# Optimization experiments

Hardware: AMD Instinct MI355X
Metric: run time of the kernel (lower is better)

## Reference

```python
import jax, jax.numpy as jnp
import numpy as np
from jax import lax

BT, ST, NT = 32, 8, 1024
CH = [128, 64, 32, 16, 8]
DIL = [1, 2, 4, 8, 16]
K = 5
EPS = 1e-5


def setup_inputs() -> dict:
    key = jax.random.key(0)
    ks = jax.random.split(key, 32)
    inp = {}
    inp["x"] = jax.random.normal(ks[0], (BT, ST, CH[0], NT), jnp.float32)
    nt_out = NT * 32  # 5 x2 upsamples
    inp["targets"] = jax.random.uniform(ks[1], (BT, 3, nt_out, ST), dtype=jnp.float32)
    for i in range(4):
        inp[f"w{i}"] = jax.random.normal(ks[2 + i], (CH[i + 1], CH[i], K), jnp.float32) * 0.05
        inp[f"g{i}"] = 1.0 + 0.1 * jax.random.normal(ks[6 + i], (CH[i + 1],), jnp.float32)
        inp[f"b{i}"] = 0.1 * jax.random.normal(ks[10 + i], (CH[i + 1],), jnp.float32)
        inp[f"m{i}"] = 0.1 * jax.random.normal(ks[14 + i], (CH[i + 1],), jnp.float32)
        inp[f"v{i}"] = 0.5 + 0.5 * jax.random.uniform(ks[18 + i], (CH[i + 1],), dtype=jnp.float32)
    inp["w_out"] = jax.random.normal(ks[22], (3, CH[4], K), jnp.float32) * 0.05
    inp["b_out"] = jax.random.normal(ks[23], (3,), jnp.float32) * 0.05
    return inp


def _conv(x, w, d):
    # reflect-padded dilated conv1d, same length out (torch padding_mode='reflect')
    p = ((K - 1) * d + 1) // 2
    xp = jnp.pad(x, ((0, 0), (0, 0), (p, p)), mode="reflect")
    return lax.conv_general_dilated(xp, w, window_strides=(1,), padding="VALID",
                                    rhs_dilation=(d,),
                                    dimension_numbers=("NCH", "OIH", "NCH"))


def _up2(x):
    # F.interpolate(scale_factor=2, mode='linear', align_corners=False)
    L = x.shape[-1]
    coords = (jnp.arange(2 * L, dtype=jnp.float32) + 0.5) / 2.0 - 0.5
    coords = jnp.clip(coords, 0.0, L - 1.0)
    i0 = jnp.floor(coords).astype(jnp.int32)
    i1 = jnp.minimum(i0 + 1, L - 1)
    w = coords - i0.astype(jnp.float32)
    return x[..., i0] * (1.0 - w) + x[..., i1] * w


def _forward(x, targets, ws, gs, bs, ms, vs, w_out, b_out):
    h = x.reshape(BT * ST, CH[0], NT)
    for i in range(4):
        h = _conv(h, ws[i], DIL[i])
        inv = gs[i] / jnp.sqrt(vs[i] + EPS)
        h = h * inv[None, :, None] + (bs[i] - ms[i] * inv)[None, :, None]  # eval-mode BN
        h = jax.nn.relu(h)
        h = _up2(h)
    h = _conv(h, w_out, DIL[4]) + b_out[None, :, None]
    h = _up2(h)
    out = h.reshape(BT, ST, 3, h.shape[-1]).transpose(0, 2, 3, 1)  # [bt, 3, nt_out, st]
    # vectorized equivalent of the per-(i,j) Python loop counting non-all-zero targets
    mask = jnp.any(targets != 0, axis=(1, 2))  # [bt, st]
    num = jnp.sum(mask).astype(jnp.float32)
    loss = jnp.sum(-targets * jax.nn.log_softmax(out, axis=1)) / (num * targets.shape[2])
    return out, loss


def reference(x, targets, w0, w1, w2, w3, g0, g1, g2, g3, b0, b1, b2, b3,
              m0, m1, m2, m3, v0, v1, v2, v3, w_out, b_out):
    return _forward(x, targets, [w0, w1, w2, w3], [g0, g1, g2, g3],
                    [b0, b1, b2, b3], [m0, m1, m2, m3], [v0, v1, v2, v3],
                    w_out, b_out)
```

## Files before the change

### kernel.cpp

```cpp
#include <hip/hip_runtime.h>
#include <hip/hip_bf16.h>
#include <cstdint>
#include <cstddef>

#define K5 5
#define BNEPS 1e-5f

typedef __attribute__((ext_vector_type(8))) short short8v;
typedef __attribute__((ext_vector_type(4))) short short4v;
typedef __attribute__((ext_vector_type(4))) float float4v;

struct __attribute__((packed, aligned(4))) f4u { float4v v; };

__device__ inline float bf2f(short s) {
    __hip_bfloat16 h = *(__hip_bfloat16*)&s;
    return __bfloat162float(h);
}
__device__ inline short f2bf(float f) {
    __hip_bfloat16 h = __float2bfloat16(f);
    return *(short*)&h;
}

template<int CIN, int COUT, int MROWS, int KPAD>
__device__ inline void wprep_body(const float* __restrict__ w,
                                  short* __restrict__ wb, int blk, int tid) {
    int idx = blk * 256 + tid;
    if (idx >= MROWS * KPAD) return;
    int co = idx / KPAD, kk = idx - co * KPAD;
    int tap = kk / CIN, ci = kk & (CIN - 1);
    float v = (co < COUT && tap < K5) ? w[((size_t)co * CIN + ci) * K5 + tap] : 0.f;
    wb[idx] = f2bf(v);
}

__global__ __launch_bounds__(256) void wprep_all_ker(
    const float* __restrict__ w0, const float* __restrict__ w1,
    const float* __restrict__ w2, const float* __restrict__ w3,
    const float* __restrict__ w4,
    short* __restrict__ wb0, short* __restrict__ wb1, short* __restrict__ wb2,
    short* __restrict__ wb3, short* __restrict__ wb4) {
    int b = blockIdx.x, t = threadIdx.x;
    if (b < 160)      wprep_body<128, 64, 64, 640>(w0, wb0, b, t);
    else if (b < 200) wprep_body<64, 32, 32, 320>(w1, wb1, b - 160, t);
    else if (b < 210) wprep_body<32, 16, 16, 160>(w2, wb2, b - 200, t);
    else if (b < 216) wprep_body<16, 8, 16, 96>(w3, wb3, b - 210, t);
    else              wprep_body<8, 3, 16, 64>(w4, wb4, b - 216, t);
}

template<int CIN, int COUT, int DIL, int LOUT, int T_TILE, int WT,
         bool HAS_BN, int IN_MODE, int OUT_MODE>
__global__ __launch_bounds__(256) void conv_ker(
    const void* __restrict__ in_, const short* __restrict__ wb,
    const float* __restrict__ gg, const float* __restrict__ bb,
    const float* __restrict__ mm, const float* __restrict__ vv,
    void* __restrict__ out_)
{
    constexpr int P = 2 * DIL;
    constexpr int XT = T_TILE + 4 * DIL;
    constexpr int ROWW = CIN + 8;
    constexpr int K = CIN * K5;
    constexpr int KPAD = ((K + 31) / 32) * 32;
    constexpr int NSTEP = KPAD / 32;
    constexpr int WCOT = (COUT + 15) / 16;
    constexpr int TN = T_TILE / (16 * WT);
    constexpr int LIN = LOUT;
    constexpr int LIN_BASE = (IN_MODE == 1) ? (LOUT / 2) : LOUT;
    static_assert(T_TILE % (16 * WT) == 0, "tile split");

    __shared__ short sx[XT * ROWW];
    __shared__ float ssc[COUT], ssh[COUT];

    const int n = blockIdx.x;
    const int t0 = blockIdx.y * T_TILE;
    const int tid = threadIdx.x;

    if (tid < COUT) {
        if constexpr (HAS_BN) {
            float inv = gg[tid] * rsqrtf(vv[tid] + BNEPS);
            ssc[tid] = inv;
            ssh[tid] = bb[tid] - mm[tid] * inv;
        } else {
            ssc[tid] = 1.f;
            ssh[tid] = bb[tid];
        }
    }

    if constexpr (IN_MODE == 0) {
        static_assert(XT % 4 == 0, "XT mult of 4");
        constexpr int T4 = XT / 4;
        constexpr int NITEM = T4 * (CIN / 8);
        const float* in = (const float*)in_;
        for (int uidx = tid; uidx < NITEM; uidx += 256) {
            int t4 = uidx % T4;
            int ci0 = (uidx / T4) * 8;
            const int u0 = t0 - P + 4 * t4;
            const float* base = in + ((size_t)n * CIN + ci0) * LIN_BASE;
            short8v rows[4];
            bool fast = (u0 >= 0) && (u0 + 3 <= LIN - 1);
            if (fast) {
#pragma unroll
                for (int j = 0; j < 8; ++j) {
                    f4u xv = *(const f4u*)(base + (size_t)j * LIN_BASE + u0);
#pragma unroll
                    for (int r = 0; r < 4; ++r) rows[r][j] = f2bf(xv.v[r]);
                }
            } else {
#pragma unroll
                for (int r = 0; r < 4; ++r) {
                    int u = u0 + r;
                    u = (u < 0) ? -u : u;
                    u = (u >= LIN) ? (2 * (LIN - 1) - u) : u;
#pragma unroll
                    for (int j = 0; j < 8; ++j)
                        rows[r][j] = f2bf(base[(size_t)j * LIN_BASE + u]);
                }
            }
            short* dst = sx + (4 * t4) * ROWW + ci0;
            *(short8v*)(dst) = rows[0];
            *(short8v*)(dst + ROWW) = rows[1];
            *(short8v*)(dst + 2 * ROWW) = rows[2];
            *(short8v*)(dst + 3 * ROWW) = rows[3];
        }
    } else {
        constexpr int CPR = CIN / 8;
        const short* inb = (const short*)in_ + (size_t)n * LIN_BASE * CIN;
        for (int uidx = tid; uidx < XT * CPR; uidx += 256) {
            int ci0 = (uidx % CPR) * 8;
            int t = uidx / CPR;
            int u = t0 - P + t;
            u = (u < 0) ? -u : u;
            u = (u >= LIN) ? (2 * (LIN - 1) - u) : u;
            int i = u >> 1;
            int ia, ib; float wa, wbw;
            if (u & 1) { ia = i; ib = (i + 1 < LIN_BASE) ? i + 1 : LIN_BASE - 1; wa = 0.75f; wbw = 0.25f; }
            else if (i == 0) { ia = 0; ib = 0; wa = 1.0f; wbw = 0.0f; }
            else { ia = i - 1; ib = i; wa = 0.25f; wbw = 0.75f; }
            short8v va = *(const short8v*)(inb + (size_t)ia * CIN + ci0);
            short8v vb = *(const short8v*)(inb + (size_t)ib * CIN + ci0);
            short8v pack;
#pragma unroll
            for (int j = 0; j < 8; ++j) {
                short sa = va[j], sb = vb[j];
                pack[j] = f2bf(wa * bf2f(sa) + wbw * bf2f(sb));
            }
            *(short8v*)(sx + t * ROWW + ci0) = pack;
        }
    }
    __syncthreads();

    const int wvi = tid >> 6;
    const int lane = tid & 63;
    const int ln = lane & 15;
    const int q = lane >> 4;
    const int tw = wvi * (TN * 16);

    float4v acc[WCOT][TN];
#pragma unroll
    for (int c = 0; c < WCOT; ++c)
#pragma unroll
        for (int j = 0; j < TN; ++j)
            acc[c][j] = (float4v){0.f, 0.f, 0.f, 0.f};

    const short* arow[WCOT];
#pragma unroll
    for (int c = 0; c < WCOT; ++c)
        arow[c] = wb + ((size_t)(c * 16 + ln)) * KPAD + q * 8;

    short8v acur[WCOT], anx[WCOT];
#pragma unroll
    for (int c = 0; c < WCOT; ++c)
        acur[c] = *(const short8v*)(arow[c]);

#pragma unroll 1
    for (int s = 0; s < NSTEP; ++s) {
        if (s + 1 < NSTEP) {
#pragma unroll
            for (int c = 0; c < WCOT; ++c)
                anx[c] = *(const short8v*)(arow[c] + (s + 1) * 32);
        }
        const int kk = s * 32 + q * 8;
        int tap = kk / CIN;
        const int ci0 = kk & (CIN - 1);
        if constexpr (KPAD != K) {
            tap = (tap < K5) ? tap : (K5 - 1);
        }
        short8v b[TN];
#pragma unroll
        for (int j = 0; j < TN; ++j)
            b[j] = *(const short8v*)(sx + (tw + j * 16 + ln + tap * DIL) * ROWW + ci0);
        if constexpr (KPAD != K) {
            if (kk >= K) {
                short8v z = {0, 0, 0, 0, 0, 0, 0, 0};
#pragma unroll
                for (int j = 0; j < TN; ++j) b[j] = z;
            }
        }
#pragma unroll
        for (int c = 0; c < WCOT; ++c)
#pragma unroll
            for (int j = 0; j < TN; ++j)
                acc[c][j] = __builtin_amdgcn_mfma_f32_16x16x32_bf16(acur[c], b[j], acc[c][j], 0, 0, 0);
#pragma unroll
        for (int c = 0; c < WCOT; ++c)
            acur[c] = anx[c];
    }

    if constexpr (OUT_MODE == 0) {
        short* ob = (short*)out_ + ((size_t)n * LOUT + t0 + tw) * COUT;
#pragma unroll
        for (int c = 0; c < WCOT; ++c)
#pragma unroll
            for (int j = 0; j < TN; ++j) {
                if ((COUT % 16 == 0) || (q * 4 + 3 < COUT)) {
                    float4v v = acc[c][j];
                    short4v pk;
#pragma unroll
                    for (int r = 0; r < 4; ++r) {
                        int co = c * 16 + q * 4 + r;
                        float val = v[r] * ssc[co] + ssh[co];
                        if constexpr (HAS_BN) val = fmaxf(val, 0.f);
                        pk[r] = f2bf(val);
                    }
                    *(short4v*)(ob + (size_t)(j * 16 + ln) * COUT + c * 16 + q * 4) = pk;
                }
            }
    } else {
        float* ob = (float*)out_ + (size_t)n * COUT * LOUT + t0 + tw + ln;
#pragma unroll
        for (int c = 0; c < WCOT; ++c)
#pragma unroll
            for (int j = 0; j < TN; ++j) {
                float4v v = acc[c][j];
#pragma unroll
                for (int r = 0; r < 4; ++r) {
                    int co = c * 16 + q * 4 + r;
                    if ((COUT % 16 == 0) || co < COUT) {
                        float val = v[r] * ssc[co] + ssh[co];
                        if constexpr (HAS_BN) val = fmaxf(val, 0.f);
                        ob[(size_t)co * LOUT + j * 16] = val;
                    }
                }
            }
    }
}

__global__ __launch_bounds__(256) void up_loss_ker(
    const float* __restrict__ h4, const float* __restrict__ targets,
    float* __restrict__ out, float* __restrict__ loss_sum, int* __restrict__ flags)
{
    constexpr int L = 16384, LO = 32768;
    const int bt = blockIdx.x;
    const int t0 = blockIdx.y * 256;
    const int tid = threadIdx.x;
    const int i0 = t0 >> 1;

    __shared__ float sh[3 * 8 * 132];
    __shared__ int snz[8];
    __shared__ float swv[4];

    {
        const bool interior = (i0 >= 1) && (i0 + 130 <= L - 1);
        for (int idx = tid; idx < 24 * 33; idx += 256) {
            int row = idx / 33;
            int qd = idx - row * 33;
            int c = row >> 3, s = row & 7;
            int nn = bt * 8 + s;
            const float* src = h4 + ((size_t)nn * 3 + c) * L;
            int bi0 = i0 - 1 + 4 * qd;
            float4v v;
            if (interior) {
                v = ((const f4u*)(src + bi0))->v;
            } else {
#pragma unroll
                for (int k = 0; k < 4; ++k) {
                    int bi = bi0 + k;
                    bi = bi < 0 ? 0 : (bi > L - 1 ? L - 1 : bi);
                    v[k] = src[bi];
                }
            }
            *(float4v*)(sh + row * 132 + 4 * qd) = v;
        }
    }
    if (tid < 8) snz[tid] = 0;
    __syncthreads();

    const int tl = tid >> 1;
    const int st4 = (tid & 1) * 4;

    float lsum = 0.f;
    int nzm = 0;
#pragma unroll
    for (int rr = 0; rr < 2; ++rr) {
        int t = t0 + rr * 128 + tl;
        int li = (t >> 1) - i0 + 1;
        float o[3][4];
#pragma unroll
        for (int c = 0; c < 3; ++c)
#pragma unroll
            for (int s = 0; s < 4; ++s) {
                const float* row = sh + ((c << 3) + st4 + s) * 132;
                float v;
                if (t & 1) v = 0.75f * row[li] + 0.25f * row[li + 1];
                else       v = 0.25f * row[li - 1] + 0.75f * row[li];
                o[c][s] = v;
            }
        float tg[3][4];
#pragma unroll
        for (int c = 0; c < 3; ++c) {
            size_t obase = (((size_t)bt * 3 + c) * LO + t) * 8 + st4;
            float4v ov = { o[c][0], o[c][1], o[c][2], o[c][3] };
            *(float4v*)(out + obase) = ov;
            float4v tv = *(const float4v*)(targets + obase);
            tg[c][0] = tv[0]; tg[c][1] = tv[1]; tg[c][2] = tv[2]; tg[c][3] = tv[3];
        }
#pragma unroll
        for (int s = 0; s < 4; ++s) {
            float a0 = o[0][s], a1 = o[1][s], a2 = o[2][s];
            float mx = fmaxf(a0, fmaxf(a1, a2));
            float e0 = __expf(a0 - mx), e1 = __expf(a1 - mx), e2 = __expf(a2 - mx);
            float lse = mx + __logf(e0 + e1 + e2);
            lsum += tg[0][s] * (lse - a0) + tg[1][s] * (lse - a1) + tg[2][s] * (lse - a2);
            if ((tg[0][s] != 0.f) | (tg[1][s] != 0.f) | (tg[2][s] != 0.f)) nzm |= 1 << s;
        }
    }
    if (nzm) {
#pragma unroll
        for (int s = 0; s < 4; ++s) if (nzm & (1 << s)) snz[st4 + s] = 1;
    }

#pragma unroll
    for (int off = 32; off > 0; off >>= 1) lsum += __shfl_down(lsum, off, 64);
    if ((tid & 63) == 0) swv[tid >> 6] = lsum;
    __syncthreads();
    if (tid == 0) atomicAdd(loss_sum, swv[0] + swv[1] + swv[2] + swv[3]);
    if (tid < 8 && snz[tid]) atomicOr(&flags[bt * 8 + tid], 1);
}

__global__ __launch_bounds__(256) void finalize_ker(
    const int* __restrict__ flags, const float* __restrict__ loss_sum,
    float* __restrict__ out_loss)
{
    __shared__ int s[256];
    s[threadIdx.x] = flags[threadIdx.x] ? 1 : 0;
    __syncthreads();
    for (int off = 128; off > 0; off >>= 1) {
        if (threadIdx.x < off) s[threadIdx.x] += s[threadIdx.x + off];
        __syncthreads();
    }
    if (threadIdx.x == 0) out_loss[0] = loss_sum[0] / ((float)s[0] * 32768.0f);
}

extern "C" void kernel_launch(void* const* d_in, const int* in_sizes, int n_in,
                              void* d_out, int out_size, void* d_ws, size_t ws_size,
                              hipStream_t stream)
{
    const float* x  = (const float*)d_in[0];
    const float* tg = (const float*)d_in[1];
    const float* w0 = (const float*)d_in[2];
    const float* g0 = (const float*)d_in[3];
    const float* b0 = (const float*)d_in[4];
    const float* m0 = (const float*)d_in[5];
    const float* v0 = (const float*)d_in[6];
    const float* w1 = (const float*)d_in[7];
    const float* g1 = (const float*)d_in[8];
    const float* b1 = (const float*)d_in[9];
    const float* m1 = (const float*)d_in[10];
    const float* v1 = (const float*)d_in[11];
    const float* w2 = (const float*)d_in[12];
    const float* g2 = (const float*)d_in[13];
    const float* b2 = (const float*)d_in[14];
    const float* m2 = (const float*)d_in[15];
    const float* v2 = (const float*)d_in[16];
    const float* w3 = (const float*)d_in[17];
    const float* g3 = (const float*)d_in[18];
    const float* b3 = (const float*)d_in[19];
    const float* m3 = (const float*)d_in[20];
    const float* v3 = (const float*)d_in[21];
    const float* w_out = (const float*)d_in[22];
    const float* b_out = (const float*)d_in[23];
    float* outp = (float*)d_out;

    char* ws = (char*)d_ws;
    int* flags = (int*)ws;
    float* loss_sum = (float*)(ws + 1024);
    short* wb0 = (short*)(ws + 4096);
    short* wb1 = (short*)(ws + 86016);
    short* wb2 = (short*)(ws + 106496);
    short* wb3 = (short*)(ws + 111616);
    short* wb4 = (short*)(ws + 114688);
    const size_t BUF_OFF = 131072;
    const size_t BUFN = (size_t)16777216;
    float* bufA = (float*)(ws + BUF_OFF);
    float* bufB = (ws_size >= BUF_OFF + 2 * BUFN * 4)
                      ? (bufA + BUFN)
                      : (float*)d_out;

    hipMemsetAsync(d_ws, 0, 4096, stream);

    wprep_all_ker<<<220, 256, 0, stream>>>(w0, w1, w2, w3, w_out,
                                           wb0, wb1, wb2, wb3, wb4);

    conv_ker<128, 64, 1, 1024, 128, 4, true, 0, 0>
        <<<dim3(256, 8), 256, 0, stream>>>(x, wb0, g0, b0, m0, v0, bufA);
    conv_ker<64, 32, 2, 2048, 128, 4, true, 1, 0>
        <<<dim3(256, 16), 256, 0, stream>>>(bufA, wb1, g1, b1, m1, v1, bufB);
    conv_ker<32, 16, 4, 4096, 256, 4, true, 1, 0>
        <<<dim3(256, 16), 256, 0, stream>>>(bufB, wb2, g2, b2, m2, v2, bufA);
    conv_ker<16, 8, 8, 8192, 256, 4, true, 1, 0>
        <<<dim3(256, 32), 256, 0, stream>>>(bufA, wb3, g3, b3, m3, v3, bufB);
    conv_ker<8, 3, 16, 16384, 256, 4, false, 1, 1>
        <<<dim3(256, 64), 256, 0, stream>>>(bufB, wb4, b_out, b_out, b_out, b_out, bufA);
    up_loss_ker<<<dim3(32, 128), 256, 0, stream>>>(bufA, tg, outp, loss_sum, flags);
    finalize_ker<<<1, 256, 0, stream>>>(flags, loss_sum, outp + (size_t)(out_size - 1));
}
```

Before: 561.7 us.

## Split conv waves across output-channel groups, enlarge time tiles, preload weights

Adds a WCO template parameter so the four waves of a block can be split between time and output-channel groups. The first two layers use a 2x2 split, which shrinks each wave's accumulator set and lets it cover more time positions. Time tiles are enlarged for layers 1-4 so fewer blocks recompute the dilated halo. Short K loops now load all weight fragments up front, and long loops prefetch two steps ahead. The cost is larger LDS tiles and more registers per wave, which can lower occupancy, and the CIN=8 row stride is padded to 24.

Result: faster. 511.0 us (-9.0%).

```diff
diff --git a/kernel.cpp b/kernel.cpp
--- a/kernel.cpp
+++ b/kernel.cpp
@@ -46,7 +46,7 @@
     else              wprep_body<8, 3, 16, 64>(w4, wb4, b - 216, t);
 }
 
-template<int CIN, int COUT, int DIL, int LOUT, int T_TILE, int WT,
+template<int CIN, int COUT, int DIL, int LOUT, int T_TILE, int WT, int WCO,
          bool HAS_BN, int IN_MODE, int OUT_MODE>
 __global__ __launch_bounds__(256) void conv_ker(
     const void* __restrict__ in_, const short* __restrict__ wb,
@@ -56,14 +56,17 @@
 {
     constexpr int P = 2 * DIL;
     constexpr int XT = T_TILE + 4 * DIL;
-    constexpr int ROWW = CIN + 8;
+    constexpr int ROWW = (CIN == 8) ? 24 : (CIN + 8);
     constexpr int K = CIN * K5;
     constexpr int KPAD = ((K + 31) / 32) * 32;
     constexpr int NSTEP = KPAD / 32;
-    constexpr int WCOT = (COUT + 15) / 16;
+    constexpr int MT = (COUT + 15) / 16;
+    constexpr int CT = MT / WCO;
     constexpr int TN = T_TILE / (16 * WT);
     constexpr int LIN = LOUT;
     constexpr int LIN_BASE = (IN_MODE == 1) ? (LOUT / 2) : LOUT;
+    static_assert(WT * WCO == 4, "4 waves");
+    static_assert(MT % WCO == 0, "co split");
     static_assert(T_TILE % (16 * WT) == 0, "tile split");
 
     __shared__ short sx[XT * ROWW];
@@ -151,63 +154,98 @@
     const int lane = tid & 63;
     const int ln = lane & 15;
     const int q = lane >> 4;
-    const int tw = wvi * (TN * 16);
-
-    float4v acc[WCOT][TN];
-#pragma unroll
-    for (int c = 0; c < WCOT; ++c)
+    const int tg = wvi % WT;
+    const int cg = wvi / WT;
+    const int tw = tg * (TN * 16);
+
+    float4v acc[CT][TN];
+#pragma unroll
+    for (int c = 0; c < CT; ++c)
 #pragma unroll
         for (int j = 0; j < TN; ++j)
             acc[c][j] = (float4v){0.f, 0.f, 0.f, 0.f};
 
-    const short* arow[WCOT];
-#pragma unroll
-    for (int c = 0; c < WCOT; ++c)
-        arow[c] = wb + ((size_t)(c * 16 + ln)) * KPAD + q * 8;
-
-    short8v acur[WCOT], anx[WCOT];
-#pragma unroll
-    for (int c = 0; c < WCOT; ++c)
-        acur[c] = *(const short8v*)(arow[c]);
-
+    const short* arow[CT];
+#pragma unroll
+    for (int c = 0; c < CT; ++c)
+        arow[c] = wb + ((size_t)((cg * CT + c) * 16 + ln)) * KPAD + q * 8;
+
+    if constexpr (NSTEP <= 6) {
+        short8v aall[NSTEP][CT];
+#pragma unroll
+        for (int s = 0; s < NSTEP; ++s)
+#pragma unroll
+            for (int c = 0; c < CT; ++c)
+                aall[s][c] = *(const short8v*)(arow[c] + s * 32);
+#pragma unroll
+        for (int s = 0; s < NSTEP; ++s) {
+            const int kk = s * 32 + q * 8;
+            int tap = kk / CIN;
+            const int ci0 = kk & (CIN - 1);
+            if constexpr (KPAD != K) {
+                tap = (tap < K5) ? tap : (K5 - 1);
+            }
+            short8v b[TN];
+#pragma unroll
+            for (int j = 0; j < TN; ++j)
+                b[j] = *(const short8v*)(sx + (tw + j * 16 + ln + tap * DIL) * ROWW + ci0);
+            if constexpr (KPAD != K) {
+                if (kk >= K) {
+                    short8v z = {0, 0, 0, 0, 0, 0, 0, 0};
+#pragma unroll
+                    for (int j = 0; j < TN; ++j) b[j] = z;
+                }
+            }
+#pragma unroll
+            for (int c = 0; c < CT; ++c)
+#pragma unroll
+                for (int j = 0; j < TN; ++j)
+                    acc[c][j] = __builtin_amdgcn_mfma_f32_16x16x32_bf16(aall[s][c], b[j], acc[c][j], 0, 0, 0);
+        }
+    } else {
+        short8v a0[CT], a1[CT], a2[CT];
+#pragma unroll
+        for (int c = 0; c < CT; ++c) a0[c] = *(const short8v*)(arow[c]);
+#pragma unroll
+        for (int c = 0; c < CT; ++c) a1[c] = *(const short8v*)(arow[c] + 32);
 #pragma unroll 1
-    for (int s = 0; s < NSTEP; ++s) {
-        if (s + 1 < NSTEP) {
-#pragma unroll
-            for (int c = 0; c < WCOT; ++c)
-                anx[c] = *(const short8v*)(arow[c] + (s + 1) * 32);
-        }
-        const int kk = s * 32 + q * 8;
-        int tap = kk / CIN;
-        const int ci0 = kk & (CIN - 1);
-        if constexpr (KPAD != K) {
-            tap = (tap < K5) ? tap : (K5 - 1);
-        }
-        short8v b[TN];
-#pragma unroll
-        for (int j = 0; j < TN; ++j)
-            b[j] = *(const short8v*)(sx + (tw + j * 16 + ln + tap * DIL) * ROWW + ci0);
-        if constexpr (KPAD != K) {
-            if (kk >= K) {
-                short8v z = {0, 0, 0, 0, 0, 0, 0, 0};
-#pragma unroll
-                for (int j = 0; j < TN; ++j) b[j] = z;
-            }
-        }
-#pragma unroll
-        for (int c = 0; c < WCOT; ++c)
+        for (int s = 0; s < NSTEP; ++s) {
+            if (s + 2 < NSTEP) {
+#pragma unroll
+                for (int c = 0; c < CT; ++c)
+                    a2[c] = *(const short8v*)(arow[c] + (s + 2) * 32);
+            }
+            const int kk = s * 32 + q * 8;
+            int tap = kk / CIN;
+            const int ci0 = kk & (CIN - 1);
+            if constexpr (KPAD != K) {
+                tap = (tap < K5) ? tap : (K5 - 1);
+            }
+            short8v b[TN];
 #pragma unroll
             for (int j = 0; j < TN; ++j)
-                acc[c][j] = __builtin_amdgcn_mfma_f32_16x16x32_bf16(acur[c], b[j], acc[c][j], 0, 0, 0);
-#pragma unroll
-        for (int c = 0; c < WCOT; ++c)
-            acur[c] = anx[c];
+                b[j] = *(const short8v*)(sx + (tw + j * 16 + ln + tap * DIL) * ROWW + ci0);
+            if constexpr (KPAD != K) {
+                if (kk >= K) {
+                    short8v z = {0, 0, 0, 0, 0, 0, 0, 0};
+#pragma unroll
+                    for (int j = 0; j < TN; ++j) b[j] = z;
+                }
+            }
+#pragma unroll
+            for (int c = 0; c < CT; ++c)
+#pragma unroll
+                for (int j = 0; j < TN; ++j)
+                    acc[c][j] = __builtin_amdgcn_mfma_f32_16x16x32_bf16(a0[c], b[j], acc[c][j], 0, 0, 0);
+#pragma unroll
+            for (int c = 0; c < CT; ++c) { a0[c] = a1[c]; a1[c] = a2[c]; }
+        }
     }
 
     if constexpr (OUT_MODE == 0) {
         short* ob = (short*)out_ + ((size_t)n * LOUT + t0 + tw) * COUT;
 #pragma unroll
-        for (int c = 0; c < WCOT; ++c)
+        for (int c = 0; c < CT; ++c)
 #pragma unroll
             for (int j = 0; j < TN; ++j) {
                 if ((COUT % 16 == 0) || (q * 4 + 3 < COUT)) {
@@ -215,24 +253,24 @@
                     short4v pk;
 #pragma unroll
                     for (int r = 0; r < 4; ++r) {
-                        int co = c * 16 + q * 4 + r;
+                        int co = (cg * CT + c) * 16 + q * 4 + r;
                         float val = v[r] * ssc[co] + ssh[co];
                         if constexpr (HAS_BN) val = fmaxf(val, 0.f);
                         pk[r] = f2bf(val);
                     }
-                    *(short4v*)(ob + (size_t)(j * 16 + ln) * COUT + c * 16 + q * 4) = pk;
+                    *(short4v*)(ob + (size_t)(j * 16 + ln) * COUT + (cg * CT + c) * 16 + q * 4) = pk;
                 }
             }
     } else {
         float* ob = (float*)out_ + (size_t)n * COUT * LOUT + t0 + tw + ln;
 #pragma unroll
-        for (int c = 0; c < WCOT; ++c)
+        for (int c = 0; c < CT; ++c)
 #pragma unroll
             for (int j = 0; j < TN; ++j) {
                 float4v v = acc[c][j];
 #pragma unroll
                 for (int r = 0; r < 4; ++r) {
-                    int co = c * 16 + q * 4 + r;
+                    int co = (cg * CT + c) * 16 + q * 4 + r;
                     if ((COUT % 16 == 0) || co < COUT) {
                         float val = v[r] * ssc[co] + ssh[co];
                         if constexpr (HAS_BN) val = fmaxf(val, 0.f);
@@ -399,16 +437,16 @@
     wprep_all_ker<<<220, 256, 0, stream>>>(w0, w1, w2, w3, w_out,
                                            wb0, wb1, wb2, wb3, wb4);
 
-    conv_ker<128, 64, 1, 1024, 128, 4, true, 0, 0>
+    conv_ker<128, 64, 1, 1024, 128, 2, 2, true, 0, 0>
         <<<dim3(256, 8), 256, 0, stream>>>(x, wb0, g0, b0, m0, v0, bufA);
-    conv_ker<64, 32, 2, 2048, 128, 4, true, 1, 0>
-        <<<dim3(256, 16), 256, 0, stream>>>(bufA, wb1, g1, b1, m1, v1, bufB);
-    conv_ker<32, 16, 4, 4096, 256, 4, true, 1, 0>
-        <<<dim3(256, 16), 256, 0, stream>>>(bufB, wb2, g2, b2, m2, v2, bufA);
-    conv_ker<16, 8, 8, 8192, 256, 4, true, 1, 0>
-        <<<dim3(256, 32), 256, 0, stream>>>(bufA, wb3, g3, b3, m3, v3, bufB);
-    conv_ker<8, 3, 16, 16384, 256, 4, false, 1, 1>
-        <<<dim3(256, 64), 256, 0, stream>>>(bufB, wb4, b_out, b_out, b_out, b_out, bufA);
+    conv_ker<64, 32, 2, 2048, 256, 2, 2, true, 1, 0>
+        <<<dim3(256, 8), 256, 0, stream>>>(bufA, wb1, g1, b1, m1, v1, bufB);
+    conv_ker<32, 16, 4, 4096, 512, 4, 1, true, 1, 0>
+        <<<dim3(256, 8), 256, 0, stream>>>(bufB, wb2, g2, b2, m2, v2, bufA);
+    conv_ker<16, 8, 8, 8192, 512, 4, 1, true, 1, 0>
+        <<<dim3(256, 16), 256, 0, stream>>>(bufA, wb3, g3, b3, m3, v3, bufB);
+    conv_ker<8, 3, 16, 16384, 512, 4, 1, false, 1, 1>
+        <<<dim3(256, 32), 256, 0, stream>>>(bufB, wb4, b_out, b_out, b_out, b_out, bufA);
     up_loss_ker<<<dim3(32, 128), 256, 0, stream>>>(bufA, tg, outp, loss_sum, flags);
     finalize_ker<<<1, 256, 0, stream>>>(flags, loss_sum, outp + (size_t)(out_size - 1));
 }
```
